# Optimization experiments

Measured on AMD Instinct MI355X. Metric: run time of the kernel, lower is better.

## Reference

```python
import jax, jax.numpy as jnp
import numpy as np

EPS = 1e-06  # min_gamma_value

def spectral_function(eigvals):
    # reciprocal spectral function: f(lambda) = 1 / lambda (lambda >= EPS by construction)
    return 1.0 / eigvals

def setup_inputs() -> dict:
    key = jax.random.key(0)
    x = jax.random.normal(key, (4, 64, 16, 128, 128), dtype=jnp.float32)  # [B, C, K, H, W]
    return {"x": x}

def reference(x):
    # [B, C, K, H, W] -> [B, H, W, K, C]
    m = jnp.transpose(x, (0, 3, 4, 2, 1))
    K = m.shape[-2]
    # per-pixel KxK Gram matrix, regularized
    sym = jnp.einsum('bhwkc,bhwlc->bhwkl', m, m) + EPS * jnp.eye(K, dtype=m.dtype)
    eigvals, eigvecs = jnp.linalg.eigh(sym)          # eigvals [B,H,W,K], eigvecs [B,H,W,K,K]
    f = spectral_function(eigvals)                    # elementwise spectral map
    # V diag(f) V^T
    out = jnp.einsum('bhwik,bhwk,bhwjk->bhwij', eigvecs, f, eigvecs)
    return out
```

## Files before the change

### kernel.cpp

```cpp
#include <hip/hip_runtime.h>
#include <utility>


#define EPSR 1e-6f

__device__ __host__ constexpr int rowof(int t) {
    int i = 0;
    while ((i + 1) * (i + 2) / 2 <= t) ++i;
    return i;
}
__device__ __host__ constexpr int colof(int t) { return t - rowof(t) * (rowof(t) + 1) / 2; }

__device__ __forceinline__ constexpr int tidx(int i, int j) {
    return i * (i + 1) / 2 + j;
}

#define GLOAD_LDS16(gp, lp)                                                       \
    __builtin_amdgcn_global_load_lds(                                             \
        (const __attribute__((address_space(1))) void*)(gp),                      \
        (__attribute__((address_space(3))) void*)(lp), 16, 0, 0)


template<int P>
__device__ __forceinline__ void fma_pair(const float (&m)[16], float& a) {
    a = fmaf(m[rowof(P)], m[colof(P)], a);
}

template<int G, int... TT>
__device__ __forceinline__ void fma_group(const float (&m)[16], float (&acc)[34],
                                          std::integer_sequence<int, TT...>) {
    (fma_pair<G * 34 + TT>(m, acc[TT]), ...);
}

template<int G>
__device__ __forceinline__ void chunk_fma4(const float* __restrict__ buf, int lane,
                                           float (&acc)[34]) {
    #pragma unroll
    for (int cs = 0; cs < 4; ++cs) {
        float m[16];
        #pragma unroll
        for (int k = 0; k < 16; ++k) m[k] = buf[(cs * 16 + k) * 64 + lane];
        fma_group<G>(m, acc, std::make_integer_sequence<int, 34>{});
    }
}

template<int P>
__device__ __forceinline__ void store_tri_pair(float* __restrict__ tri, int lane, float v) {
    constexpr bool diag = (rowof(P) == colof(P));
    tri[P * 67 + lane] = diag ? (v + EPSR) : v;
}

template<int G, int... TT>
__device__ __forceinline__ void store_tri_group(float* __restrict__ tri, int lane,
                                                const float (&acc)[34],
                                                std::integer_sequence<int, TT...>) {
    (store_tri_pair<G * 34 + TT>(tri, lane, acc[TT]), ...);
}


union SMem {
    float stage[2][4096];
    float tri[136 * 67];
};

__global__ __launch_bounds__(256, 4)
void fused_gram_inv(const float* __restrict__ x, float* __restrict__ out) {
    __shared__ __align__(16) SMem sm;

    const int tid = threadIdx.x;
    const int lane = tid & 63;
    const int wv = tid >> 6;
    const int p0 = blockIdx.x * 64;
    const int b = blockIdx.x >> 8;
    const int hw0 = p0 & 16383;

    const float* gbase = x + (size_t)b * 16777216 + hw0
                           + (size_t)(lane >> 4) * 16384 + (size_t)(lane & 15) * 4;

    float acc[34];
    #pragma unroll
    for (int t = 0; t < 34; ++t) acc[t] = 0.0f;

    auto STAGE = [&](int bufi, int c0) {
        #pragma unroll
        for (int q = 0; q < 4; ++q) {
            GLOAD_LDS16(gbase + (size_t)(c0 + wv) * 262144 + (size_t)(q * 4) * 16384,
                        &sm.stage[bufi][(wv * 16 + q * 4) * 64]);
        }
    };

    STAGE(0, 0);
    for (int t = 0; t < 16; ++t) {
        __syncthreads();
        if (t < 15) STAGE((t + 1) & 1, 4 * (t + 1));
        const float* buf = sm.stage[t & 1];
        switch (wv) {
            case 0:  chunk_fma4<0>(buf, lane, acc); break;
            case 1:  chunk_fma4<1>(buf, lane, acc); break;
            case 2:  chunk_fma4<2>(buf, lane, acc); break;
            default: chunk_fma4<3>(buf, lane, acc); break;
        }
    }
    __syncthreads();

    switch (wv) {
        case 0:  store_tri_group<0>(sm.tri, lane, acc, std::make_integer_sequence<int, 34>{}); break;
        case 1:  store_tri_group<1>(sm.tri, lane, acc, std::make_integer_sequence<int, 34>{}); break;
        case 2:  store_tri_group<2>(sm.tri, lane, acc, std::make_integer_sequence<int, 34>{}); break;
        default: store_tri_group<3>(sm.tri, lane, acc, std::make_integer_sequence<int, 34>{}); break;
    }
    __syncthreads();

    if (wv == 0) {
        float* lp = &sm.tri[lane];
        #define SL(t) lp[(t) * 67]

        #pragma unroll
        for (int j = 0; j < 16; ++j) {
            float rj[16];
            #pragma unroll
            for (int q = 0; q < j; ++q) rj[q] = SL(tidx(j, q));
            float d = SL(tidx(j, j));
            #pragma unroll
            for (int q = 0; q < j; ++q) d = fmaf(-rj[q], rj[q], d);
            const float invd = 1.0f / sqrtf(d);
            SL(tidx(j, j)) = invd;
            #pragma unroll
            for (int i = j + 1; i < 16; ++i) {
                float v = SL(tidx(i, j));
                #pragma unroll
                for (int q = 0; q < j; ++q) v = fmaf(-SL(tidx(i, q)), rj[q], v);
                SL(tidx(i, j)) = v * invd;
            }
        }

        #pragma unroll
        for (int j = 0; j < 16; ++j) {
            float col[16];
            col[j] = SL(tidx(j, j));
            #pragma unroll
            for (int i = j + 1; i < 16; ++i) {
                float sum = SL(tidx(i, j)) * col[j];
                #pragma unroll
                for (int q = j + 1; q < i; ++q)
                    sum = fmaf(SL(tidx(i, q)), col[q], sum);
                const float mii = SL(tidx(i, i));
                const float mij = -mii * sum;
                col[i] = mij;
                SL(tidx(i, j)) = mij;
            }
        }

        #pragma unroll
        for (int j = 0; j < 16; ++j) {
            float cj[16];
            #pragma unroll
            for (int q = j; q < 16; ++q) cj[q] = SL(tidx(q, j));
            #pragma unroll
            for (int i = j; i < 16; ++i) {
                float sum = 0.0f;
                if (i == j) {
                    #pragma unroll
                    for (int q = j; q < 16; ++q) sum = fmaf(cj[q], cj[q], sum);
                } else {
                    #pragma unroll
                    for (int q = i; q < 16; ++q) sum = fmaf(SL(tidx(q, i)), cj[q], sum);
                }
                SL(tidx(i, j)) = sum;
            }
        }
        #undef SL
    }
    __syncthreads();

    const int e = tid;
    const int i = e >> 4, j = e & 15;
    const int hi = i > j ? i : j;
    const int lo = i + j - hi;
    const int trow = hi * (hi + 1) / 2 + lo;
    float* gout = out + (size_t)p0 * 256;
    #pragma unroll 8
    for (int a = 0; a < 64; ++a) {
        gout[(size_t)a * 256 + e] = sm.tri[trow * 67 + a];
    }
}

extern "C" void kernel_launch(void* const* d_in, const int* in_sizes, int n_in,
                              void* d_out, int out_size, void* d_ws, size_t ws_size,
                              hipStream_t stream) {
    const float* x = (const float*)d_in[0];
    float* out = (float*)d_out;
    hipLaunchKernelGGL(fused_gram_inv, dim3(1024), dim3(256), 0, stream, x, out);
}
```

Baseline: 84.63 us.

## Halve block to two waves and keep Cholesky inversion in registers

Blocks shrink from 256 to 128 threads, so each of the two waves accumulates 68 Gram entries instead of 34 and issues twice the staged loads. The single-wave Cholesky, triangular inverse and product phase now loads the whole 136-entry triangle into registers once, instead of reading and writing LDS for every element. The goal is to cut LDS traffic in the serial inversion and lower the share of idle waves during it. The cost is much higher register pressure (68 accumulators plus a 136-float array), which risks spills and lower occupancy, and fewer waves are left to hide memory latency.

```diff
diff --git a/kernel.cpp b/kernel.cpp
--- a/kernel.cpp
+++ b/kernel.cpp
@@ -27,20 +27,20 @@
 }
 
 template<int G, int... TT>
-__device__ __forceinline__ void fma_group(const float (&m)[16], float (&acc)[34],
+__device__ __forceinline__ void fma_group(const float (&m)[16], float (&acc)[68],
                                           std::integer_sequence<int, TT...>) {
-    (fma_pair<G * 34 + TT>(m, acc[TT]), ...);
+    (fma_pair<G * 68 + TT>(m, acc[TT]), ...);
 }
 
 template<int G>
 __device__ __forceinline__ void chunk_fma4(const float* __restrict__ buf, int lane,
-                                           float (&acc)[34]) {
+                                           float (&acc)[68]) {
     #pragma unroll
     for (int cs = 0; cs < 4; ++cs) {
         float m[16];
         #pragma unroll
         for (int k = 0; k < 16; ++k) m[k] = buf[(cs * 16 + k) * 64 + lane];
-        fma_group<G>(m, acc, std::make_integer_sequence<int, 34>{});
+        fma_group<G>(m, acc, std::make_integer_sequence<int, 68>{});
     }
 }
 
@@ -52,9 +52,9 @@
 
 template<int G, int... TT>
 __device__ __forceinline__ void store_tri_group(float* __restrict__ tri, int lane,
-                                                const float (&acc)[34],
+                                                const float (&acc)[68],
                                                 std::integer_sequence<int, TT...>) {
-    (store_tri_pair<G * 34 + TT>(tri, lane, acc[TT]), ...);
+    (store_tri_pair<G * 68 + TT>(tri, lane, acc[TT]), ...);
 }
 
 
@@ -63,7 +63,7 @@
     float tri[136 * 67];
 };
 
-__global__ __launch_bounds__(256, 4)
+__global__ __launch_bounds__(128, 2)
 void fused_gram_inv(const float* __restrict__ x, float* __restrict__ out) {
     __shared__ __align__(16) SMem sm;
 
@@ -77,15 +77,19 @@
     const float* gbase = x + (size_t)b * 16777216 + hw0
                            + (size_t)(lane >> 4) * 16384 + (size_t)(lane & 15) * 4;
 
-    float acc[34];
+    float acc[68];
     #pragma unroll
-    for (int t = 0; t < 34; ++t) acc[t] = 0.0f;
+    for (int t = 0; t < 68; ++t) acc[t] = 0.0f;
 
     auto STAGE = [&](int bufi, int c0) {
         #pragma unroll
-        for (int q = 0; q < 4; ++q) {
-            GLOAD_LDS16(gbase + (size_t)(c0 + wv) * 262144 + (size_t)(q * 4) * 16384,
-                        &sm.stage[bufi][(wv * 16 + q * 4) * 64]);
+        for (int s = 0; s < 2; ++s) {
+            const int cs = wv + 2 * s;
+            #pragma unroll
+            for (int q = 0; q < 4; ++q) {
+                GLOAD_LDS16(gbase + (size_t)(c0 + cs) * 262144 + (size_t)(q * 4) * 16384,
+                            &sm.stage[bufi][(cs * 16 + q * 4) * 64]);
+            }
         }
     };
 
@@ -94,94 +98,79 @@
         __syncthreads();
         if (t < 15) STAGE((t + 1) & 1, 4 * (t + 1));
         const float* buf = sm.stage[t & 1];
-        switch (wv) {
-            case 0:  chunk_fma4<0>(buf, lane, acc); break;
-            case 1:  chunk_fma4<1>(buf, lane, acc); break;
-            case 2:  chunk_fma4<2>(buf, lane, acc); break;
-            default: chunk_fma4<3>(buf, lane, acc); break;
-        }
+        if (wv == 0) chunk_fma4<0>(buf, lane, acc);
+        else         chunk_fma4<1>(buf, lane, acc);
     }
     __syncthreads();
 
-    switch (wv) {
-        case 0:  store_tri_group<0>(sm.tri, lane, acc, std::make_integer_sequence<int, 34>{}); break;
-        case 1:  store_tri_group<1>(sm.tri, lane, acc, std::make_integer_sequence<int, 34>{}); break;
-        case 2:  store_tri_group<2>(sm.tri, lane, acc, std::make_integer_sequence<int, 34>{}); break;
-        default: store_tri_group<3>(sm.tri, lane, acc, std::make_integer_sequence<int, 34>{}); break;
-    }
+    if (wv == 0) store_tri_group<0>(sm.tri, lane, acc, std::make_integer_sequence<int, 68>{});
+    else         store_tri_group<1>(sm.tri, lane, acc, std::make_integer_sequence<int, 68>{});
     __syncthreads();
 
     if (wv == 0) {
-        float* lp = &sm.tri[lane];
-        #define SL(t) lp[(t) * 67]
+        float s[136];
+        #pragma unroll
+        for (int t = 0; t < 136; ++t) s[t] = sm.tri[t * 67 + lane];
 
         #pragma unroll
         for (int j = 0; j < 16; ++j) {
-            float rj[16];
+            float d = s[tidx(j, j)];
             #pragma unroll
-            for (int q = 0; q < j; ++q) rj[q] = SL(tidx(j, q));
-            float d = SL(tidx(j, j));
-            #pragma unroll
-            for (int q = 0; q < j; ++q) d = fmaf(-rj[q], rj[q], d);
+            for (int q = 0; q < j; ++q) d = fmaf(-s[tidx(j, q)], s[tidx(j, q)], d);
             const float invd = 1.0f / sqrtf(d);
-            SL(tidx(j, j)) = invd;
+            s[tidx(j, j)] = invd;
             #pragma unroll
             for (int i = j + 1; i < 16; ++i) {
-                float v = SL(tidx(i, j));
+                float v = s[tidx(i, j)];
                 #pragma unroll
-                for (int q = 0; q < j; ++q) v = fmaf(-SL(tidx(i, q)), rj[q], v);
-                SL(tidx(i, j)) = v * invd;
+                for (int q = 0; q < j; ++q) v = fmaf(-s[tidx(i, q)], s[tidx(j, q)], v);
+                s[tidx(i, j)] = v * invd;
             }
         }
 
         #pragma unroll
         for (int j = 0; j < 16; ++j) {
-            float col[16];
-            col[j] = SL(tidx(j, j));
             #pragma unroll
             for (int i = j + 1; i < 16; ++i) {
-                float sum = SL(tidx(i, j)) * col[j];
+                float sum = s[tidx(i, j)] * s[tidx(j, j)];
                 #pragma unroll
                 for (int q = j + 1; q < i; ++q)
-                    sum = fmaf(SL(tidx(i, q)), col[q], sum);
-                const float mii = SL(tidx(i, i));
-                const float mij = -mii * sum;
-                col[i] = mij;
-                SL(tidx(i, j)) = mij;
+                    sum = fmaf(s[tidx(i, q)], s[tidx(q, j)], sum);
+                s[tidx(i, j)] = -s[tidx(i, i)] * sum;
             }
         }
 
         #pragma unroll
         for (int j = 0; j < 16; ++j) {
-            float cj[16];
-            #pragma unroll
-            for (int q = j; q < 16; ++q) cj[q] = SL(tidx(q, j));
             #pragma unroll
             for (int i = j; i < 16; ++i) {
                 float sum = 0.0f;
-                if (i == j) {
-                    #pragma unroll
-                    for (int q = j; q < 16; ++q) sum = fmaf(cj[q], cj[q], sum);
-                } else {
-                    #pragma unroll
-                    for (int q = i; q < 16; ++q) sum = fmaf(SL(tidx(q, i)), cj[q], sum);
-                }
-                SL(tidx(i, j)) = sum;
+                #pragma unroll
+                for (int q = i; q < 16; ++q)
+                    sum = fmaf(s[tidx(q, i)], s[tidx(q, j)], sum);
+                s[tidx(i, j)] = sum;
             }
         }
-        #undef SL
+
+        #pragma unroll
+        for (int t = 0; t < 136; ++t) sm.tri[t * 67 + lane] = s[t];
     }
     __syncthreads();
 
-    const int e = tid;
-    const int i = e >> 4, j = e & 15;
-    const int hi = i > j ? i : j;
-    const int lo = i + j - hi;
-    const int trow = hi * (hi + 1) / 2 + lo;
+    const int e0 = tid;
+    const int e1 = tid + 128;
+    const int i0 = e0 >> 4, j0 = e0 & 15;
+    const int h0 = i0 > j0 ? i0 : j0, l0 = i0 + j0 - h0;
+    const int trow0 = h0 * (h0 + 1) / 2 + l0;
+    const int i1 = e1 >> 4, j1 = e1 & 15;
+    const int h1 = i1 > j1 ? i1 : j1, l1 = i1 + j1 - h1;
+    const int trow1 = h1 * (h1 + 1) / 2 + l1;
+
     float* gout = out + (size_t)p0 * 256;
     #pragma unroll 8
     for (int a = 0; a < 64; ++a) {
-        gout[(size_t)a * 256 + e] = sm.tri[trow * 67 + a];
+        gout[(size_t)a * 256 + e0] = sm.tri[trow0 * 67 + a];
+        gout[(size_t)a * 256 + e1] = sm.tri[trow1 * 67 + a];
     }
 }
 
@@ -190,5 +179,5 @@
                               hipStream_t stream) {
     const float* x = (const float*)d_in[0];
     float* out = (float*)d_out;
-    hipLaunchKernelGGL(fused_gram_inv, dim3(1024), dim3(256), 0, stream, x, out);
+    hipLaunchKernelGGL(fused_gram_inv, dim3(1024), dim3(128), 0, stream, x, out);
 }
```

Measured after the change: 78.34 us. -7.4%, faster.
